# Kernel optimization log

Hardware: AMD Instinct MI355X
Metric: run time of the kernel (lower is better)

The kernel has to match this reference:

```python
import jax, jax.numpy as jnp
import numpy as np

HEAD_DIM = 128
SCALE = 1.0 / np.sqrt(HEAD_DIM).astype(np.float32)


def setup_inputs() -> dict:
    key = jax.random.key(0)
    kq, kk, kv = jax.random.split(key, 3)
    B, S, H, KVH, D = 2, 2048, 32, 8, HEAD_DIM
    q = jax.random.normal(kq, (B, S, H, D), dtype=jnp.float32)
    k = jax.random.normal(kk, (B, S, KVH, D), dtype=jnp.float32)
    v = jax.random.normal(kv, (B, S, KVH, D), dtype=jnp.float32)
    return {"q": q, "k": k, "v": v}


def reference(q, k, v):
    # q: [B,S,H,D]; k,v: [B,S,KVH,D]
    B, S, H, D = q.shape
    kvh = k.shape[2]
    if kvh != H:
        rep = H // kvh
        # repeat_interleave along head dim (GQA -> MHA expansion)
        k = jnp.repeat(k, rep, axis=2)
        v = jnp.repeat(v, rep, axis=2)
    # scores: [B,H,S,S]
    scores = jnp.einsum("bqhd,bkhd->bhqk", q, k) * SCALE
    causal_mask = jnp.triu(jnp.ones((S, S), dtype=bool), k=1)
    scores = jnp.where(causal_mask, -jnp.inf, scores)
    attn = jax.nn.softmax(scores, axis=-1)
    # output back to [B,S,H,D]
    out = jnp.einsum("bhqk,bkhd->bqhd", attn, v)
    return out
```

## Files before the change

kernel.cpp:

```cpp
#include <hip/hip_runtime.h>
#include <hip/hip_bf16.h>
#include <stdint.h>

#define B_    2
#define S_    2048
#define H_    32
#define KVH_  8
#define D_    128
#define NBLK  512
#define NTOT_ 34

typedef __bf16 bf16x8 __attribute__((ext_vector_type(8)));
typedef unsigned short u16x8 __attribute__((ext_vector_type(8)));
typedef unsigned int u32x4 __attribute__((ext_vector_type(4)));
typedef float f32x4 __attribute__((ext_vector_type(4)));

__device__ constexpr float SCALE_LOG2E = 0.08838834764831845f * 1.4426950408889634f;
__device__ constexpr float DEFER_LOG2  = 11.0f;

__device__ __forceinline__ unsigned short f2bf(float f) {
    unsigned int u = __builtin_bit_cast(unsigned int, f);
    u = (u + 0x7FFFu + ((u >> 16) & 1u)) >> 16;
    return (unsigned short)u;
}

__device__ __forceinline__ unsigned int cvt_pk_bf16(float lo, float hi) {
    unsigned int r;
    asm("v_cvt_pk_bf16_f32 %0, %1, %2" : "=v"(r) : "v"(lo), "v"(hi));
    return r;
}

__device__ __forceinline__ void gload16(const unsigned short* gsrc, unsigned short* ldst) {
    __builtin_amdgcn_global_load_lds(
        (const __attribute__((address_space(1))) unsigned int*)gsrc,
        (__attribute__((address_space(3))) unsigned int*)ldst,
        16, 0, 0);
}

__global__ __launch_bounds__(256) void prepass(const float* __restrict__ k,
                                               const float* __restrict__ v,
                                               unsigned short* __restrict__ kbuf,
                                               unsigned short* __restrict__ vbuf) {
    if (blockIdx.x < 2048) {
        int tid = blockIdx.x * 256 + threadIdx.x;
        int l   = tid & 63;
        int ch  = (tid >> 6) & 3;
        int kb  = (tid >> 8) & 127;
        int kvh = (tid >> 15) & 7;
        int b   = tid >> 18;
        int s   = kb * 16 + (l & 15);
        int d0  = ch * 32 + (l >> 4) * 8;
        const float* src = k + (((size_t)b * S_ + s) * KVH_ + kvh) * D_ + d0;
        float4 x = ((const float4*)src)[0];
        float4 y = ((const float4*)src)[1];
        u16x8 o;
        o[0] = f2bf(x.x); o[1] = f2bf(x.y); o[2] = f2bf(x.z); o[3] = f2bf(x.w);
        o[4] = f2bf(y.x); o[5] = f2bf(y.y); o[6] = f2bf(y.z); o[7] = f2bf(y.w);
        *(u16x8*)(kbuf + ((size_t)(((b * KVH_ + kvh) * 128 + kb) * 4 + ch) * 64 + l) * 8) = o;
    } else {
        __shared__ float tile[32][130];
        int bid = blockIdx.x - 2048;
        int vb  = bid & 63;
        int kvh = (bid >> 6) & 7;
        int b   = bid >> 9;
        int t   = threadIdx.x;

        int s   = t >> 3;
        int c16 = (t & 7) * 16;
        const float* src = v + (((size_t)b * S_ + vb * 32 + s) * KVH_ + kvh) * D_ + c16;
        #pragma unroll
        for (int j = 0; j < 4; ++j) {
            float4 x = ((const float4*)src)[j];
            tile[s][c16 + 4 * j + 0] = x.x; tile[s][c16 + 4 * j + 1] = x.y;
            tile[s][c16 + 4 * j + 2] = x.z; tile[s][c16 + 4 * j + 3] = x.w;
        }
        __syncthreads();

        #pragma unroll
        for (int i = 0; i < 2; ++i) {
            int ci = t + i * 256;
            int mt = ci >> 6, l = ci & 63, c = l & 15, g = l >> 4;
            u16x8 o;
            #pragma unroll
            for (int j = 0; j < 8; ++j) o[j] = f2bf(tile[g * 8 + j][mt * 16 + c]);
            *(u16x8*)(vbuf + ((size_t)(((b * KVH_ + kvh) * 64 + vb) * 8 + mt) * 64 + l) * 8) = o;
        }
    }
}

__global__ __launch_bounds__(256, 2)
void attn_fwd(const float* __restrict__ q,
              const unsigned short* __restrict__ kbuf,
              const unsigned short* __restrict__ vbuf,
              float* __restrict__ out)
{
    int pid = blockIdx.x;
    int lid = (pid & 7) * (NBLK / 8) + (pid >> 3);
    int p   = lid & 7;
    int bh  = lid >> 3;
    int b   = bh >> 5, h = bh & 31, kvh = h >> 2;
    const int qtA = 15 - p;
    const int NTA = 2 * qtA + 2;
    const int qtB = p;

    const int tid = threadIdx.x, wave = tid >> 6, lane = tid & 63;
    const int c = lane & 15, g = lane >> 4;

    __shared__ __align__(16) unsigned short ldsK[2][8192];
    __shared__ __align__(16) unsigned short ldsV[2][8192];

    const unsigned short* kfb = kbuf + (size_t)(b * KVH_ + kvh) * (S_ * D_);
    const unsigned short* vfb = vbuf + (size_t)(b * KVH_ + kvh) * (S_ * D_);

    const int addr0 = (c + 16 * ((2 * g) & 3)) * 4;
    const int addr1 = (c + 16 * ((2 * g + 1) & 3)) * 4;
    const bool ghi = (g >= 2);

    auto kvt = [&](int u) { return (u < NTA) ? u : (u - NTA); };
    auto stageK = [&](int u) {
        const unsigned short* ks = kfb + (size_t)kvt(u) * 8192;
        unsigned short* ld = &ldsK[u & 1][0];
        #pragma unroll
        for (int i = 0; i < 4; ++i) {
            int seg = wave * 4 + i;
            gload16(ks + seg * 512 + lane * 8, ld + seg * 512);
        }
    };
    auto stageV = [&](int u) {
        const unsigned short* vs = vfb + (size_t)kvt(u) * 8192;
        unsigned short* ld = &ldsV[u & 1][0];
        #pragma unroll
        for (int i = 0; i < 4; ++i) {
            int seg = wave * 4 + i;
            gload16(vs + seg * 512 + lane * 8, ld + seg * 512);
        }
    };

    stageK(0);
    asm volatile("s_waitcnt vmcnt(0)" ::: "memory");
    __builtin_amdgcn_s_barrier();
    asm volatile("" ::: "memory");

    auto run_tile = [&](int qt, int u0, int NT) {
        const int q0w = qt * 128 + wave * 32;

        bf16x8 qf[2][4];
        #pragma unroll
        for (int m = 0; m < 2; ++m) {
            const float* qp = q + ((size_t)b * S_ + q0w + m * 16 + c) * (H_ * D_) + h * D_ + g * 8;
            #pragma unroll
            for (int ch = 0; ch < 4; ++ch) {
                float4 a  = ((const float4*)(qp + ch * 32))[0];
                float4 bb = ((const float4*)(qp + ch * 32))[1];
                u16x8 tt;
                tt[0] = f2bf(a.x * SCALE_LOG2E);  tt[1] = f2bf(a.y * SCALE_LOG2E);
                tt[2] = f2bf(a.z * SCALE_LOG2E);  tt[3] = f2bf(a.w * SCALE_LOG2E);
                tt[4] = f2bf(bb.x * SCALE_LOG2E); tt[5] = f2bf(bb.y * SCALE_LOG2E);
                tt[6] = f2bf(bb.z * SCALE_LOG2E); tt[7] = f2bf(bb.w * SCALE_LOG2E);
                qf[m][ch] = __builtin_bit_cast(bf16x8, tt);
            }
        }

        f32x4 acc[2][8];
        #pragma unroll
        for (int m = 0; m < 2; ++m)
            #pragma unroll
            for (int mt = 0; mt < 8; ++mt) acc[m][mt] = (f32x4){0.f, 0.f, 0.f, 0.f};
        float mrun[2], lsum[2];
        #pragma unroll
        for (int m = 0; m < 2; ++m) { mrun[m] = -INFINITY; lsum[m] = 0.f; }

        u32x4 pfA[2][2], pfB[2][2];

        auto body = [&](int u, int it, int NT_, auto& pfW, auto& pfR, int ODD) {
            if (u + 1 < NTOT_) stageK(u + 1);
            stageV(u);
            const bool act = (it < NT_ - 1) || (wave >= 2);
            const int k0 = it * 64;
            f32x4 sv[2][4];

            if (act) {
                __builtin_amdgcn_s_setprio(1);
                #pragma unroll
                for (int t2 = 0; t2 < 4; ++t2) {
                    bf16x8 kf[4];
                    #pragma unroll
                    for (int ch = 0; ch < 4; ++ch)
                        kf[ch] = *(const bf16x8*)&ldsK[ODD][(t2 * 4 + ch) * 512 + lane * 8];
                    sv[0][t2] = (f32x4){0.f, 0.f, 0.f, 0.f};
                    sv[1][t2] = (f32x4){0.f, 0.f, 0.f, 0.f};
                    #pragma unroll
                    for (int ch = 0; ch < 4; ++ch) {
                        sv[0][t2] = __builtin_amdgcn_mfma_f32_16x16x32_bf16(kf[ch], qf[0][ch], sv[0][t2], 0, 0, 0);
                        sv[1][t2] = __builtin_amdgcn_mfma_f32_16x16x32_bf16(kf[ch], qf[1][ch], sv[1][t2], 0, 0, 0);
                    }
                }
                __builtin_amdgcn_s_setprio(0);
            }

            if (it > 0) {
                __builtin_amdgcn_s_setprio(1);
                #pragma unroll
                for (int kc = 0; kc < 2; ++kc) {
                    bf16x8 pb0 = __builtin_bit_cast(bf16x8, pfR[0][kc]);
                    bf16x8 pb1 = __builtin_bit_cast(bf16x8, pfR[1][kc]);
                    #pragma unroll
                    for (int mt = 0; mt < 8; ++mt) {
                        bf16x8 vf = *(const bf16x8*)&ldsV[ODD ^ 1][(kc * 8 + mt) * 512 + lane * 8];
                        acc[0][mt] = __builtin_amdgcn_mfma_f32_16x16x32_bf16(vf, pb0, acc[0][mt], 0, 0, 0);
                        acc[1][mt] = __builtin_amdgcn_mfma_f32_16x16x32_bf16(vf, pb1, acc[1][mt], 0, 0, 0);
                    }
                }
                __builtin_amdgcn_s_setprio(0);
            }

            if (act) {
                #pragma unroll
                for (int m = 0; m < 2; ++m) {
                    if (k0 + 63 > q0w + m * 16) {
                        #pragma unroll
                        for (int t2 = 0; t2 < 4; ++t2)
                            #pragma unroll
                            for (int r = 0; r < 4; ++r)
                                if (k0 + 16 * t2 + 4 * g + r > q0w + m * 16 + c) sv[m][t2][r] = -INFINITY;
                    }
                }

                float lm[2];
                #pragma unroll
                for (int m = 0; m < 2; ++m) {
                    float a0 = fmaxf(fmaxf(sv[m][0][0], sv[m][0][1]), fmaxf(sv[m][0][2], sv[m][0][3]));
                    float a1 = fmaxf(fmaxf(sv[m][1][0], sv[m][1][1]), fmaxf(sv[m][1][2], sv[m][1][3]));
                    float a2 = fmaxf(fmaxf(sv[m][2][0], sv[m][2][1]), fmaxf(sv[m][2][2], sv[m][2][3]));
                    float a3 = fmaxf(fmaxf(sv[m][3][0], sv[m][3][1]), fmaxf(sv[m][3][2], sv[m][3][3]));
                    lm[m] = fmaxf(fmaxf(a0, a1), fmaxf(a2, a3));
                }
                bool ok = (lm[0] <= mrun[0] + DEFER_LOG2) && (lm[1] <= mrun[1] + DEFER_LOG2);
                if (!__all(ok)) {
                    #pragma unroll
                    for (int m = 0; m < 2; ++m) {
                        float mx = lm[m];
                        mx = fmaxf(mx, __shfl_xor(mx, 16));
                        mx = fmaxf(mx, __shfl_xor(mx, 32));
                        float mn = fmaxf(mrun[m], mx);
                        float al = exp2f(mrun[m] - mn);
                        mrun[m] = mn;
                        lsum[m] *= al;
                        #pragma unroll
                        for (int mt = 0; mt < 8; ++mt) {
                            acc[m][mt][0] *= al; acc[m][mt][1] *= al;
                            acc[m][mt][2] *= al; acc[m][mt][3] *= al;
                        }
                    }
                }

                #pragma unroll
                for (int m = 0; m < 2; ++m) {
                    float pvv[4][4];
                    #pragma unroll
                    for (int t2 = 0; t2 < 4; ++t2)
                        #pragma unroll
                        for (int r = 0; r < 4; ++r)
                            pvv[t2][r] = exp2f(sv[m][t2][r] - mrun[m]);
                    float s01 = (pvv[0][0] + pvv[0][1]) + (pvv[0][2] + pvv[0][3])
                              + (pvv[1][0] + pvv[1][1]) + (pvv[1][2] + pvv[1][3]);
                    float s23 = (pvv[2][0] + pvv[2][1]) + (pvv[2][2] + pvv[2][3])
                              + (pvv[3][0] + pvv[3][1]) + (pvv[3][2] + pvv[3][3]);
                    lsum[m] += s01 + s23;
                    #pragma unroll
                    for (int kc = 0; kc < 2; ++kc) {
                        unsigned int we0 = cvt_pk_bf16(pvv[2 * kc][0], pvv[2 * kc][1]);
                        unsigned int we1 = cvt_pk_bf16(pvv[2 * kc][2], pvv[2 * kc][3]);
                        unsigned int wo0 = cvt_pk_bf16(pvv[2 * kc + 1][0], pvv[2 * kc + 1][1]);
                        unsigned int wo1 = cvt_pk_bf16(pvv[2 * kc + 1][2], pvv[2 * kc + 1][3]);
                        u32x4 W;
                        {
                            int x0 = __builtin_amdgcn_ds_bpermute(addr0, (int)we0);
                            int x1 = __builtin_amdgcn_ds_bpermute(addr0, (int)wo0);
                            W[0] = (unsigned int)(ghi ? x1 : x0);
                            int x2 = __builtin_amdgcn_ds_bpermute(addr0, (int)we1);
                            int x3 = __builtin_amdgcn_ds_bpermute(addr0, (int)wo1);
                            W[1] = (unsigned int)(ghi ? x3 : x2);
                            int x4 = __builtin_amdgcn_ds_bpermute(addr1, (int)we0);
                            int x5 = __builtin_amdgcn_ds_bpermute(addr1, (int)wo0);
                            W[2] = (unsigned int)(ghi ? x5 : x4);
                            int x6 = __builtin_amdgcn_ds_bpermute(addr1, (int)we1);
                            int x7 = __builtin_amdgcn_ds_bpermute(addr1, (int)wo1);
                            W[3] = (unsigned int)(ghi ? x7 : x6);
                        }
                        pfW[m][kc] = W;
                    }
                }
            }

            asm volatile("s_waitcnt vmcnt(0)" ::: "memory");
            __builtin_amdgcn_s_barrier();
            asm volatile("" ::: "memory");
        };

        for (int it = 0; it < NT; it += 2) {
            body(u0 + it,     it,     NT, pfA, pfB, 0);
            body(u0 + it + 1, it + 1, NT, pfB, pfA, 1);
        }

        if (wave >= 2) {
            #pragma unroll
            for (int kc = 0; kc < 2; ++kc) {
                bf16x8 pb0 = __builtin_bit_cast(bf16x8, pfB[0][kc]);
                bf16x8 pb1 = __builtin_bit_cast(bf16x8, pfB[1][kc]);
                #pragma unroll
                for (int mt = 0; mt < 8; ++mt) {
                    bf16x8 vf = *(const bf16x8*)&ldsV[1][(kc * 8 + mt) * 512 + lane * 8];
                    acc[0][mt] = __builtin_amdgcn_mfma_f32_16x16x32_bf16(vf, pb0, acc[0][mt], 0, 0, 0);
                    acc[1][mt] = __builtin_amdgcn_mfma_f32_16x16x32_bf16(vf, pb1, acc[1][mt], 0, 0, 0);
                }
            }
        }

        #pragma unroll
        for (int m = 0; m < 2; ++m) {
            lsum[m] += __shfl_xor(lsum[m], 16);
            lsum[m] += __shfl_xor(lsum[m], 32);
        }
        #pragma unroll
        for (int m = 0; m < 2; ++m) {
            float linv = 1.0f / lsum[m];
            float* ob = out + ((size_t)b * S_ + q0w + m * 16 + c) * (H_ * D_) + h * D_;
            #pragma unroll
            for (int mt = 0; mt < 8; ++mt) {
                float4 o;
                o.x = acc[m][mt][0] * linv; o.y = acc[m][mt][1] * linv;
                o.z = acc[m][mt][2] * linv; o.w = acc[m][mt][3] * linv;
                *(float4*)(ob + mt * 16 + 4 * g) = o;
            }
        }
    };

    run_tile(qtA, 0, NTA);
    run_tile(qtB, NTA, NTOT_ - NTA);
}

extern "C" void kernel_launch(void* const* d_in, const int* in_sizes, int n_in,
                              void* d_out, int out_size, void* d_ws, size_t ws_size,
                              hipStream_t stream) {
    const float* q = (const float*)d_in[0];
    const float* k = (const float*)d_in[1];
    const float* v = (const float*)d_in[2];
    float* out = (float*)d_out;

    unsigned short* kbuf = (unsigned short*)d_ws;
    unsigned short* vbuf = kbuf + (size_t)B_ * KVH_ * S_ * D_;

    prepass<<<3072, 256, 0, stream>>>(k, v, kbuf, vbuf);
    attn_fwd<<<NBLK, 256, 0, stream>>>(q, kbuf, vbuf, out);
}
```

Measured before the change: 128.5 us.

## Use 512-thread blocks with 256-row query tiles instead of paired 128-row tiles

Each block now runs 8 waves over one 256-row query tile, where before it ran 4 waves over two complementary 128-row tiles. Each K/V tile staged in LDS is therefore shared by twice as many waves, and the two-tile causal load balancing gives way to a reversed block order across the two halves of the grid. Per-wave skipping of fully masked tiles (act/pact) replaces the old last-iteration rule. In exchange there is more causal imbalance inside a block, since early waves sit idle at barriers while later waves finish. The launch bounds are raised to 512 threads with 4 blocks per CU, which may constrain registers.

```diff
diff --git a/kernel.cpp b/kernel.cpp
--- a/kernel.cpp
+++ b/kernel.cpp
@@ -8,7 +8,6 @@
 #define KVH_  8
 #define D_    128
 #define NBLK  512
-#define NTOT_ 34
 
 typedef __bf16 bf16x8 __attribute__((ext_vector_type(8)));
 typedef unsigned short u16x8 __attribute__((ext_vector_type(8)));
@@ -88,23 +87,26 @@
     }
 }
 
-__global__ __launch_bounds__(256, 2)
+__global__ __launch_bounds__(512, 4)
 void attn_fwd(const float* __restrict__ q,
               const unsigned short* __restrict__ kbuf,
               const unsigned short* __restrict__ vbuf,
               float* __restrict__ out)
 {
-    int pid = blockIdx.x;
-    int lid = (pid & 7) * (NBLK / 8) + (pid >> 3);
-    int p   = lid & 7;
-    int bh  = lid >> 3;
-    int b   = bh >> 5, h = bh & 31, kvh = h >> 2;
-    const int qtA = 15 - p;
-    const int NTA = 2 * qtA + 2;
-    const int qtB = p;
+    const int pid  = blockIdx.x;
+    const int half = pid >> 8;
+    const int r    = pid & 255;
+    const int kvg  = r & 15;
+    const int hq   = (r >> 4) & 3;
+    const int j    = r >> 6;
+    const int b    = kvg >> 3, kvh = kvg & 7;
+    const int h    = kvh * 4 + hq;
+    const int qt   = half ? j : 7 - j;
+    const int NT   = 4 * qt + 4;
 
     const int tid = threadIdx.x, wave = tid >> 6, lane = tid & 63;
     const int c = lane & 15, g = lane >> 4;
+    const int q0w = qt * 256 + wave * 32;
 
     __shared__ __align__(16) unsigned short ldsK[2][8192];
     __shared__ __align__(16) unsigned short ldsV[2][8192];
@@ -116,22 +118,21 @@
     const int addr1 = (c + 16 * ((2 * g + 1) & 3)) * 4;
     const bool ghi = (g >= 2);
 
-    auto kvt = [&](int u) { return (u < NTA) ? u : (u - NTA); };
     auto stageK = [&](int u) {
-        const unsigned short* ks = kfb + (size_t)kvt(u) * 8192;
+        const unsigned short* ks = kfb + (size_t)u * 8192;
         unsigned short* ld = &ldsK[u & 1][0];
         #pragma unroll
-        for (int i = 0; i < 4; ++i) {
-            int seg = wave * 4 + i;
+        for (int i = 0; i < 2; ++i) {
+            int seg = wave * 2 + i;
             gload16(ks + seg * 512 + lane * 8, ld + seg * 512);
         }
     };
     auto stageV = [&](int u) {
-        const unsigned short* vs = vfb + (size_t)kvt(u) * 8192;
+        const unsigned short* vs = vfb + (size_t)u * 8192;
         unsigned short* ld = &ldsV[u & 1][0];
         #pragma unroll
-        for (int i = 0; i < 4; ++i) {
-            int seg = wave * 4 + i;
+        for (int i = 0; i < 2; ++i) {
+            int seg = wave * 2 + i;
             gload16(vs + seg * 512 + lane * 8, ld + seg * 512);
         }
     };
@@ -141,203 +142,197 @@
     __builtin_amdgcn_s_barrier();
     asm volatile("" ::: "memory");
 
-    auto run_tile = [&](int qt, int u0, int NT) {
-        const int q0w = qt * 128 + wave * 32;
-
-        bf16x8 qf[2][4];
-        #pragma unroll
-        for (int m = 0; m < 2; ++m) {
-            const float* qp = q + ((size_t)b * S_ + q0w + m * 16 + c) * (H_ * D_) + h * D_ + g * 8;
-            #pragma unroll
-            for (int ch = 0; ch < 4; ++ch) {
-                float4 a  = ((const float4*)(qp + ch * 32))[0];
-                float4 bb = ((const float4*)(qp + ch * 32))[1];
-                u16x8 tt;
-                tt[0] = f2bf(a.x * SCALE_LOG2E);  tt[1] = f2bf(a.y * SCALE_LOG2E);
-                tt[2] = f2bf(a.z * SCALE_LOG2E);  tt[3] = f2bf(a.w * SCALE_LOG2E);
-                tt[4] = f2bf(bb.x * SCALE_LOG2E); tt[5] = f2bf(bb.y * SCALE_LOG2E);
-                tt[6] = f2bf(bb.z * SCALE_LOG2E); tt[7] = f2bf(bb.w * SCALE_LOG2E);
-                qf[m][ch] = __builtin_bit_cast(bf16x8, tt);
-            }
-        }
-
-        f32x4 acc[2][8];
-        #pragma unroll
-        for (int m = 0; m < 2; ++m)
-            #pragma unroll
-            for (int mt = 0; mt < 8; ++mt) acc[m][mt] = (f32x4){0.f, 0.f, 0.f, 0.f};
-        float mrun[2], lsum[2];
-        #pragma unroll
-        for (int m = 0; m < 2; ++m) { mrun[m] = -INFINITY; lsum[m] = 0.f; }
-
-        u32x4 pfA[2][2], pfB[2][2];
-
-        auto body = [&](int u, int it, int NT_, auto& pfW, auto& pfR, int ODD) {
-            if (u + 1 < NTOT_) stageK(u + 1);
-            stageV(u);
-            const bool act = (it < NT_ - 1) || (wave >= 2);
-            const int k0 = it * 64;
-            f32x4 sv[2][4];
-
-            if (act) {
-                __builtin_amdgcn_s_setprio(1);
-                #pragma unroll
-                for (int t2 = 0; t2 < 4; ++t2) {
-                    bf16x8 kf[4];
-                    #pragma unroll
-                    for (int ch = 0; ch < 4; ++ch)
-                        kf[ch] = *(const bf16x8*)&ldsK[ODD][(t2 * 4 + ch) * 512 + lane * 8];
-                    sv[0][t2] = (f32x4){0.f, 0.f, 0.f, 0.f};
-                    sv[1][t2] = (f32x4){0.f, 0.f, 0.f, 0.f};
-                    #pragma unroll
-                    for (int ch = 0; ch < 4; ++ch) {
-                        sv[0][t2] = __builtin_amdgcn_mfma_f32_16x16x32_bf16(kf[ch], qf[0][ch], sv[0][t2], 0, 0, 0);
-                        sv[1][t2] = __builtin_amdgcn_mfma_f32_16x16x32_bf16(kf[ch], qf[1][ch], sv[1][t2], 0, 0, 0);
-                    }
-                }
-                __builtin_amdgcn_s_setprio(0);
-            }
-
-            if (it > 0) {
-                __builtin_amdgcn_s_setprio(1);
-                #pragma unroll
-                for (int kc = 0; kc < 2; ++kc) {
-                    bf16x8 pb0 = __builtin_bit_cast(bf16x8, pfR[0][kc]);
-                    bf16x8 pb1 = __builtin_bit_cast(bf16x8, pfR[1][kc]);
-                    #pragma unroll
-                    for (int mt = 0; mt < 8; ++mt) {
-                        bf16x8 vf = *(const bf16x8*)&ldsV[ODD ^ 1][(kc * 8 + mt) * 512 + lane * 8];
-                        acc[0][mt] = __builtin_amdgcn_mfma_f32_16x16x32_bf16(vf, pb0, acc[0][mt], 0, 0, 0);
-                        acc[1][mt] = __builtin_amdgcn_mfma_f32_16x16x32_bf16(vf, pb1, acc[1][mt], 0, 0, 0);
-                    }
-                }
-                __builtin_amdgcn_s_setprio(0);
-            }
-
-            if (act) {
-                #pragma unroll
-                for (int m = 0; m < 2; ++m) {
-                    if (k0 + 63 > q0w + m * 16) {
-                        #pragma unroll
-                        for (int t2 = 0; t2 < 4; ++t2)
-                            #pragma unroll
-                            for (int r = 0; r < 4; ++r)
-                                if (k0 + 16 * t2 + 4 * g + r > q0w + m * 16 + c) sv[m][t2][r] = -INFINITY;
-                    }
-                }
-
-                float lm[2];
-                #pragma unroll
-                for (int m = 0; m < 2; ++m) {
-                    float a0 = fmaxf(fmaxf(sv[m][0][0], sv[m][0][1]), fmaxf(sv[m][0][2], sv[m][0][3]));
-                    float a1 = fmaxf(fmaxf(sv[m][1][0], sv[m][1][1]), fmaxf(sv[m][1][2], sv[m][1][3]));
-                    float a2 = fmaxf(fmaxf(sv[m][2][0], sv[m][2][1]), fmaxf(sv[m][2][2], sv[m][2][3]));
-                    float a3 = fmaxf(fmaxf(sv[m][3][0], sv[m][3][1]), fmaxf(sv[m][3][2], sv[m][3][3]));
-                    lm[m] = fmaxf(fmaxf(a0, a1), fmaxf(a2, a3));
-                }
-                bool ok = (lm[0] <= mrun[0] + DEFER_LOG2) && (lm[1] <= mrun[1] + DEFER_LOG2);
-                if (!__all(ok)) {
-                    #pragma unroll
-                    for (int m = 0; m < 2; ++m) {
-                        float mx = lm[m];
-                        mx = fmaxf(mx, __shfl_xor(mx, 16));
-                        mx = fmaxf(mx, __shfl_xor(mx, 32));
-                        float mn = fmaxf(mrun[m], mx);
-                        float al = exp2f(mrun[m] - mn);
-                        mrun[m] = mn;
-                        lsum[m] *= al;
-                        #pragma unroll
-                        for (int mt = 0; mt < 8; ++mt) {
-                            acc[m][mt][0] *= al; acc[m][mt][1] *= al;
-                            acc[m][mt][2] *= al; acc[m][mt][3] *= al;
-                        }
-                    }
-                }
-
-                #pragma unroll
-                for (int m = 0; m < 2; ++m) {
-                    float pvv[4][4];
+    bf16x8 qf[2][4];
+    #pragma unroll
+    for (int m = 0; m < 2; ++m) {
+        const float* qp = q + ((size_t)b * S_ + q0w + m * 16 + c) * (H_ * D_) + h * D_ + g * 8;
+        #pragma unroll
+        for (int ch = 0; ch < 4; ++ch) {
+            float4 a  = ((const float4*)(qp + ch * 32))[0];
+            float4 bb = ((const float4*)(qp + ch * 32))[1];
+            u16x8 tt;
+            tt[0] = f2bf(a.x * SCALE_LOG2E);  tt[1] = f2bf(a.y * SCALE_LOG2E);
+            tt[2] = f2bf(a.z * SCALE_LOG2E);  tt[3] = f2bf(a.w * SCALE_LOG2E);
+            tt[4] = f2bf(bb.x * SCALE_LOG2E); tt[5] = f2bf(bb.y * SCALE_LOG2E);
+            tt[6] = f2bf(bb.z * SCALE_LOG2E); tt[7] = f2bf(bb.w * SCALE_LOG2E);
+            qf[m][ch] = __builtin_bit_cast(bf16x8, tt);
+        }
+    }
+
+    f32x4 acc[2][8];
+    #pragma unroll
+    for (int m = 0; m < 2; ++m)
+        #pragma unroll
+        for (int mt = 0; mt < 8; ++mt) acc[m][mt] = (f32x4){0.f, 0.f, 0.f, 0.f};
+    float mrun[2], lsum[2];
+    #pragma unroll
+    for (int m = 0; m < 2; ++m) { mrun[m] = -INFINITY; lsum[m] = 0.f; }
+
+    u32x4 pfA[2][2], pfB[2][2];
+
+    auto body = [&](int it, auto& pfW, auto& pfR, int ODD) {
+        if (it + 1 < NT) stageK(it + 1);
+        stageV(it);
+        const int k0 = it * 64;
+        const bool act  = (k0 <= q0w + 31);
+        const bool pact = (it > 0) && (k0 - 64 <= q0w + 31);
+        f32x4 sv[2][4];
+
+        if (act) {
+            __builtin_amdgcn_s_setprio(1);
+            #pragma unroll
+            for (int t2 = 0; t2 < 4; ++t2) {
+                bf16x8 kf[4];
+                #pragma unroll
+                for (int ch = 0; ch < 4; ++ch)
+                    kf[ch] = *(const bf16x8*)&ldsK[ODD][(t2 * 4 + ch) * 512 + lane * 8];
+                sv[0][t2] = (f32x4){0.f, 0.f, 0.f, 0.f};
+                sv[1][t2] = (f32x4){0.f, 0.f, 0.f, 0.f};
+                #pragma unroll
+                for (int ch = 0; ch < 4; ++ch) {
+                    sv[0][t2] = __builtin_amdgcn_mfma_f32_16x16x32_bf16(kf[ch], qf[0][ch], sv[0][t2], 0, 0, 0);
+                    sv[1][t2] = __builtin_amdgcn_mfma_f32_16x16x32_bf16(kf[ch], qf[1][ch], sv[1][t2], 0, 0, 0);
+                }
+            }
+            __builtin_amdgcn_s_setprio(0);
+        }
+
+        if (pact) {
+            __builtin_amdgcn_s_setprio(1);
+            #pragma unroll
+            for (int kc = 0; kc < 2; ++kc) {
+                bf16x8 pb0 = __builtin_bit_cast(bf16x8, pfR[0][kc]);
+                bf16x8 pb1 = __builtin_bit_cast(bf16x8, pfR[1][kc]);
+                #pragma unroll
+                for (int mt = 0; mt < 8; ++mt) {
+                    bf16x8 vf = *(const bf16x8*)&ldsV[ODD ^ 1][(kc * 8 + mt) * 512 + lane * 8];
+                    acc[0][mt] = __builtin_amdgcn_mfma_f32_16x16x32_bf16(vf, pb0, acc[0][mt], 0, 0, 0);
+                    acc[1][mt] = __builtin_amdgcn_mfma_f32_16x16x32_bf16(vf, pb1, acc[1][mt], 0, 0, 0);
+                }
+            }
+            __builtin_amdgcn_s_setprio(0);
+        }
+
+        if (act) {
+            #pragma unroll
+            for (int m = 0; m < 2; ++m) {
+                if (k0 + 63 > q0w + m * 16) {
                     #pragma unroll
                     for (int t2 = 0; t2 < 4; ++t2)
                         #pragma unroll
-                        for (int r = 0; r < 4; ++r)
-                            pvv[t2][r] = exp2f(sv[m][t2][r] - mrun[m]);
-                    float s01 = (pvv[0][0] + pvv[0][1]) + (pvv[0][2] + pvv[0][3])
-                              + (pvv[1][0] + pvv[1][1]) + (pvv[1][2] + pvv[1][3]);
-                    float s23 = (pvv[2][0] + pvv[2][1]) + (pvv[2][2] + pvv[2][3])
-                              + (pvv[3][0] + pvv[3][1]) + (pvv[3][2] + pvv[3][3]);
-                    lsum[m] += s01 + s23;
+                        for (int rr = 0; rr < 4; ++rr)
+                            if (k0 + 16 * t2 + 4 * g + rr > q0w + m * 16 + c) sv[m][t2][rr] = -INFINITY;
+                }
+            }
+
+            float lm[2];
+            #pragma unroll
+            for (int m = 0; m < 2; ++m) {
+                float a0 = fmaxf(fmaxf(sv[m][0][0], sv[m][0][1]), fmaxf(sv[m][0][2], sv[m][0][3]));
+                float a1 = fmaxf(fmaxf(sv[m][1][0], sv[m][1][1]), fmaxf(sv[m][1][2], sv[m][1][3]));
+                float a2 = fmaxf(fmaxf(sv[m][2][0], sv[m][2][1]), fmaxf(sv[m][2][2], sv[m][2][3]));
+                float a3 = fmaxf(fmaxf(sv[m][3][0], sv[m][3][1]), fmaxf(sv[m][3][2], sv[m][3][3]));
+                lm[m] = fmaxf(fmaxf(a0, a1), fmaxf(a2, a3));
+            }
+            bool ok = (lm[0] <= mrun[0] + DEFER_LOG2) && (lm[1] <= mrun[1] + DEFER_LOG2);
+            if (!__all(ok)) {
+                #pragma unroll
+                for (int m = 0; m < 2; ++m) {
+                    float mx = lm[m];
+                    mx = fmaxf(mx, __shfl_xor(mx, 16));
+                    mx = fmaxf(mx, __shfl_xor(mx, 32));
+                    float mn = fmaxf(mrun[m], mx);
+                    float al = exp2f(mrun[m] - mn);
+                    mrun[m] = mn;
+                    lsum[m] *= al;
                     #pragma unroll
-                    for (int kc = 0; kc < 2; ++kc) {
-                        unsigned int we0 = cvt_pk_bf16(pvv[2 * kc][0], pvv[2 * kc][1]);
-                        unsigned int we1 = cvt_pk_bf16(pvv[2 * kc][2], pvv[2 * kc][3]);
-                        unsigned int wo0 = cvt_pk_bf16(pvv[2 * kc + 1][0], pvv[2 * kc + 1][1]);
-                        unsigned int wo1 = cvt_pk_bf16(pvv[2 * kc + 1][2], pvv[2 * kc + 1][3]);
-                        u32x4 W;
-                        {
-                            int x0 = __builtin_amdgcn_ds_bpermute(addr0, (int)we0);
-                            int x1 = __builtin_amdgcn_ds_bpermute(addr0, (int)wo0);
-                            W[0] = (unsigned int)(ghi ? x1 : x0);
-                            int x2 = __builtin_amdgcn_ds_bpermute(addr0, (int)we1);
-                            int x3 = __builtin_amdgcn_ds_bpermute(addr0, (int)wo1);
-                            W[1] = (unsigned int)(ghi ? x3 : x2);
-                            int x4 = __builtin_amdgcn_ds_bpermute(addr1, (int)we0);
-                            int x5 = __builtin_amdgcn_ds_bpermute(addr1, (int)wo0);
-                            W[2] = (unsigned int)(ghi ? x5 : x4);
-                            int x6 = __builtin_amdgcn_ds_bpermute(addr1, (int)we1);
-                            int x7 = __builtin_amdgcn_ds_bpermute(addr1, (int)wo1);
-                            W[3] = (unsigned int)(ghi ? x7 : x6);
-                        }
-                        pfW[m][kc] = W;
+                    for (int mt = 0; mt < 8; ++mt) {
+                        acc[m][mt][0] *= al; acc[m][mt][1] *= al;
+                        acc[m][mt][2] *= al; acc[m][mt][3] *= al;
                     }
                 }
             }
 
-            asm volatile("s_waitcnt vmcnt(0)" ::: "memory");
-            __builtin_amdgcn_s_barrier();
-            asm volatile("" ::: "memory");
-        };
-
-        for (int it = 0; it < NT; it += 2) {
-            body(u0 + it,     it,     NT, pfA, pfB, 0);
-            body(u0 + it + 1, it + 1, NT, pfB, pfA, 1);
-        }
-
-        if (wave >= 2) {
-            #pragma unroll
-            for (int kc = 0; kc < 2; ++kc) {
-                bf16x8 pb0 = __builtin_bit_cast(bf16x8, pfB[0][kc]);
-                bf16x8 pb1 = __builtin_bit_cast(bf16x8, pfB[1][kc]);
-                #pragma unroll
-                for (int mt = 0; mt < 8; ++mt) {
-                    bf16x8 vf = *(const bf16x8*)&ldsV[1][(kc * 8 + mt) * 512 + lane * 8];
-                    acc[0][mt] = __builtin_amdgcn_mfma_f32_16x16x32_bf16(vf, pb0, acc[0][mt], 0, 0, 0);
-                    acc[1][mt] = __builtin_amdgcn_mfma_f32_16x16x32_bf16(vf, pb1, acc[1][mt], 0, 0, 0);
-                }
-            }
-        }
-
-        #pragma unroll
-        for (int m = 0; m < 2; ++m) {
-            lsum[m] += __shfl_xor(lsum[m], 16);
-            lsum[m] += __shfl_xor(lsum[m], 32);
-        }
-        #pragma unroll
-        for (int m = 0; m < 2; ++m) {
-            float linv = 1.0f / lsum[m];
-            float* ob = out + ((size_t)b * S_ + q0w + m * 16 + c) * (H_ * D_) + h * D_;
+            #pragma unroll
+            for (int m = 0; m < 2; ++m) {
+                float pvv[4][4];
+                #pragma unroll
+                for (int t2 = 0; t2 < 4; ++t2)
+                    #pragma unroll
+                    for (int rr = 0; rr < 4; ++rr)
+                        pvv[t2][rr] = exp2f(sv[m][t2][rr] - mrun[m]);
+                float s01 = (pvv[0][0] + pvv[0][1]) + (pvv[0][2] + pvv[0][3])
+                          + (pvv[1][0] + pvv[1][1]) + (pvv[1][2] + pvv[1][3]);
+                float s23 = (pvv[2][0] + pvv[2][1]) + (pvv[2][2] + pvv[2][3])
+                          + (pvv[3][0] + pvv[3][1]) + (pvv[3][2] + pvv[3][3]);
+                lsum[m] += s01 + s23;
+                #pragma unroll
+                for (int kc = 0; kc < 2; ++kc) {
+                    unsigned int we0 = cvt_pk_bf16(pvv[2 * kc][0], pvv[2 * kc][1]);
+                    unsigned int we1 = cvt_pk_bf16(pvv[2 * kc][2], pvv[2 * kc][3]);
+                    unsigned int wo0 = cvt_pk_bf16(pvv[2 * kc + 1][0], pvv[2 * kc + 1][1]);
+                    unsigned int wo1 = cvt_pk_bf16(pvv[2 * kc + 1][2], pvv[2 * kc + 1][3]);
+                    u32x4 W;
+                    {
+                        int x0 = __builtin_amdgcn_ds_bpermute(addr0, (int)we0);
+                        int x1 = __builtin_amdgcn_ds_bpermute(addr0, (int)wo0);
+                        W[0] = (unsigned int)(ghi ? x1 : x0);
+                        int x2 = __builtin_amdgcn_ds_bpermute(addr0, (int)we1);
+                        int x3 = __builtin_amdgcn_ds_bpermute(addr0, (int)wo1);
+                        W[1] = (unsigned int)(ghi ? x3 : x2);
+                        int x4 = __builtin_amdgcn_ds_bpermute(addr1, (int)we0);
+                        int x5 = __builtin_amdgcn_ds_bpermute(addr1, (int)wo0);
+                        W[2] = (unsigned int)(ghi ? x5 : x4);
+                        int x6 = __builtin_amdgcn_ds_bpermute(addr1, (int)we1);
+                        int x7 = __builtin_amdgcn_ds_bpermute(addr1, (int)wo1);
+                        W[3] = (unsigned int)(ghi ? x7 : x6);
+                    }
+                    pfW[m][kc] = W;
+                }
+            }
+        }
+
+        asm volatile("s_waitcnt vmcnt(0)" ::: "memory");
+        __builtin_amdgcn_s_barrier();
+        asm volatile("" ::: "memory");
+    };
+
+    for (int it = 0; it < NT; it += 2) {
+        body(it,     pfA, pfB, 0);
+        body(it + 1, pfB, pfA, 1);
+    }
+
+    if (wave >= 6) {
+        #pragma unroll
+        for (int kc = 0; kc < 2; ++kc) {
+            bf16x8 pb0 = __builtin_bit_cast(bf16x8, pfB[0][kc]);
+            bf16x8 pb1 = __builtin_bit_cast(bf16x8, pfB[1][kc]);
             #pragma unroll
             for (int mt = 0; mt < 8; ++mt) {
-                float4 o;
-                o.x = acc[m][mt][0] * linv; o.y = acc[m][mt][1] * linv;
-                o.z = acc[m][mt][2] * linv; o.w = acc[m][mt][3] * linv;
-                *(float4*)(ob + mt * 16 + 4 * g) = o;
-            }
-        }
-    };
-
-    run_tile(qtA, 0, NTA);
-    run_tile(qtB, NTA, NTOT_ - NTA);
+                bf16x8 vf = *(const bf16x8*)&ldsV[1][(kc * 8 + mt) * 512 + lane * 8];
+                acc[0][mt] = __builtin_amdgcn_mfma_f32_16x16x32_bf16(vf, pb0, acc[0][mt], 0, 0, 0);
+                acc[1][mt] = __builtin_amdgcn_mfma_f32_16x16x32_bf16(vf, pb1, acc[1][mt], 0, 0, 0);
+            }
+        }
+    }
+
+    #pragma unroll
+    for (int m = 0; m < 2; ++m) {
+        lsum[m] += __shfl_xor(lsum[m], 16);
+        lsum[m] += __shfl_xor(lsum[m], 32);
+    }
+    #pragma unroll
+    for (int m = 0; m < 2; ++m) {
+        float linv = 1.0f / lsum[m];
+        float* ob = out + ((size_t)b * S_ + q0w + m * 16 + c) * (H_ * D_) + h * D_;
+        #pragma unroll
+        for (int mt = 0; mt < 8; ++mt) {
+            float4 o;
+            o.x = acc[m][mt][0] * linv; o.y = acc[m][mt][1] * linv;
+            o.z = acc[m][mt][2] * linv; o.w = acc[m][mt][3] * linv;
+            *(float4*)(ob + mt * 16 + 4 * g) = o;
+        }
+    }
 }
 
 extern "C" void kernel_launch(void* const* d_in, const int* in_sizes, int n_in,
@@ -352,5 +347,5 @@
     unsigned short* vbuf = kbuf + (size_t)B_ * KVH_ * S_ * D_;
 
     prepass<<<3072, 256, 0, stream>>>(k, v, kbuf, vbuf);
-    attn_fwd<<<NBLK, 256, 0, stream>>>(q, kbuf, vbuf, out);
-}
+    attn_fwd<<<NBLK, 512, 0, stream>>>(q, kbuf, vbuf, out);
+}
```

Measured after the change: 440.7 us. +242.9%, slower.

## Switch attention MFMAs from 16x16x32 to 32x32x16 with matching K/V layouts

Applied to the files above, without the earlier changes.

Replaces the 16x16x32 bf16 MFMA tiling with 32x32x16 MFMAs for both QK^T and PV. The prepass packing of K and V is reworked to match the new operand layout, and the P-fragment shuffle is simplified to a single lane^32 bpermute. Per-tile activity is now computed from actual causal bounds rather than a wave heuristic. The aim is fewer MFMA issues, fewer LDS reads and fewer permutes per tile, at the cost of larger accumulator register footprints that may pressure occupancy.

```diff
diff --git a/kernel.cpp b/kernel.cpp
--- a/kernel.cpp
+++ b/kernel.cpp
@@ -13,7 +13,7 @@
 typedef __bf16 bf16x8 __attribute__((ext_vector_type(8)));
 typedef unsigned short u16x8 __attribute__((ext_vector_type(8)));
 typedef unsigned int u32x4 __attribute__((ext_vector_type(4)));
-typedef float f32x4 __attribute__((ext_vector_type(4)));
+typedef float f32x16 __attribute__((ext_vector_type(16)));
 
 __device__ constexpr float SCALE_LOG2E = 0.08838834764831845f * 1.4426950408889634f;
 __device__ constexpr float DEFER_LOG2  = 11.0f;
@@ -44,46 +44,50 @@
     if (blockIdx.x < 2048) {
         int tid = blockIdx.x * 256 + threadIdx.x;
         int l   = tid & 63;
-        int ch  = (tid >> 6) & 3;
-        int kb  = (tid >> 8) & 127;
+        int ch  = (tid >> 6) & 7;
+        int kt  = (tid >> 9) & 63;
         int kvh = (tid >> 15) & 7;
-        int b   = tid >> 18;
-        int s   = kb * 16 + (l & 15);
-        int d0  = ch * 32 + (l >> 4) * 8;
+        int b   = (tid >> 18) & 1;
+        int s   = kt * 32 + (l & 31);
+        int d0  = ch * 16 + (l >> 5) * 8;
         const float* src = k + (((size_t)b * S_ + s) * KVH_ + kvh) * D_ + d0;
         float4 x = ((const float4*)src)[0];
         float4 y = ((const float4*)src)[1];
         u16x8 o;
         o[0] = f2bf(x.x); o[1] = f2bf(x.y); o[2] = f2bf(x.z); o[3] = f2bf(x.w);
         o[4] = f2bf(y.x); o[5] = f2bf(y.y); o[6] = f2bf(y.z); o[7] = f2bf(y.w);
-        *(u16x8*)(kbuf + ((size_t)(((b * KVH_ + kvh) * 128 + kb) * 4 + ch) * 64 + l) * 8) = o;
+        *(u16x8*)(kbuf + ((size_t)(((b * KVH_ + kvh) * 64 + kt) * 8 + ch) * 512 + l * 8)) = o;
     } else {
-        __shared__ float tile[32][130];
+        __shared__ float tile[64][132];
         int bid = blockIdx.x - 2048;
-        int vb  = bid & 63;
-        int kvh = (bid >> 6) & 7;
-        int b   = bid >> 9;
+        int u   = bid & 31;
+        int kvh = (bid >> 5) & 7;
+        int b   = bid >> 8;
         int t   = threadIdx.x;
 
-        int s   = t >> 3;
-        int c16 = (t & 7) * 16;
-        const float* src = v + (((size_t)b * S_ + vb * 32 + s) * KVH_ + kvh) * D_ + c16;
-        #pragma unroll
-        for (int j = 0; j < 4; ++j) {
-            float4 x = ((const float4*)src)[j];
-            tile[s][c16 + 4 * j + 0] = x.x; tile[s][c16 + 4 * j + 1] = x.y;
-            tile[s][c16 + 4 * j + 2] = x.z; tile[s][c16 + 4 * j + 3] = x.w;
+        int s  = t >> 2;
+        int cb = (t & 3) * 32;
+        const float* src = v + (((size_t)b * S_ + u * 64 + s) * KVH_ + kvh) * D_ + cb;
+        #pragma unroll
+        for (int i = 0; i < 8; ++i) {
+            float4 x = ((const float4*)src)[i];
+            tile[s][cb + 4 * i + 0] = x.x; tile[s][cb + 4 * i + 1] = x.y;
+            tile[s][cb + 4 * i + 2] = x.z; tile[s][cb + 4 * i + 3] = x.w;
         }
         __syncthreads();
 
         #pragma unroll
-        for (int i = 0; i < 2; ++i) {
-            int ci = t + i * 256;
-            int mt = ci >> 6, l = ci & 63, c = l & 15, g = l >> 4;
+        for (int i = 0; i < 4; ++i) {
+            int slot = t + 256 * i;
+            int ci = slot >> 6;
+            int l  = slot & 63;
+            int kk = ci >> 2, dt = ci & 3;
+            int h2 = l >> 5;
             u16x8 o;
             #pragma unroll
-            for (int j = 0; j < 8; ++j) o[j] = f2bf(tile[g * 8 + j][mt * 16 + c]);
-            *(u16x8*)(vbuf + ((size_t)(((b * KVH_ + kvh) * 64 + vb) * 8 + mt) * 64 + l) * 8) = o;
+            for (int j = 0; j < 8; ++j)
+                o[j] = f2bf(tile[kk * 16 + h2 * 8 + j][dt * 32 + (l & 31)]);
+            *(u16x8*)(vbuf + ((size_t)(((b * KVH_ + kvh) * 32 + u) * 16 + ci) * 512 + l * 8)) = o;
         }
     }
 }
@@ -104,17 +108,14 @@
     const int qtB = p;
 
     const int tid = threadIdx.x, wave = tid >> 6, lane = tid & 63;
-    const int c = lane & 15, g = lane >> 4;
+    const int c32 = lane & 31, hi = lane >> 5;
+    const int addrx = ((lane ^ 32) << 2);
 
     __shared__ __align__(16) unsigned short ldsK[2][8192];
     __shared__ __align__(16) unsigned short ldsV[2][8192];
 
     const unsigned short* kfb = kbuf + (size_t)(b * KVH_ + kvh) * (S_ * D_);
     const unsigned short* vfb = vbuf + (size_t)(b * KVH_ + kvh) * (S_ * D_);
-
-    const int addr0 = (c + 16 * ((2 * g) & 3)) * 4;
-    const int addr1 = (c + 16 * ((2 * g + 1) & 3)) * 4;
-    const bool ghi = (g >= 2);
 
     auto kvt = [&](int u) { return (u < NTA) ? u : (u - NTA); };
     auto stageK = [&](int u) {
@@ -144,151 +145,128 @@
     auto run_tile = [&](int qt, int u0, int NT) {
         const int q0w = qt * 128 + wave * 32;
 
-        bf16x8 qf[2][4];
-        #pragma unroll
-        for (int m = 0; m < 2; ++m) {
-            const float* qp = q + ((size_t)b * S_ + q0w + m * 16 + c) * (H_ * D_) + h * D_ + g * 8;
-            #pragma unroll
-            for (int ch = 0; ch < 4; ++ch) {
-                float4 a  = ((const float4*)(qp + ch * 32))[0];
-                float4 bb = ((const float4*)(qp + ch * 32))[1];
+        bf16x8 qf[8];
+        {
+            const float* qp = q + ((size_t)b * S_ + q0w + c32) * (H_ * D_) + h * D_ + hi * 8;
+            #pragma unroll
+            for (int ch = 0; ch < 8; ++ch) {
+                float4 a  = ((const float4*)(qp + ch * 16))[0];
+                float4 bb = ((const float4*)(qp + ch * 16))[1];
                 u16x8 tt;
                 tt[0] = f2bf(a.x * SCALE_LOG2E);  tt[1] = f2bf(a.y * SCALE_LOG2E);
                 tt[2] = f2bf(a.z * SCALE_LOG2E);  tt[3] = f2bf(a.w * SCALE_LOG2E);
                 tt[4] = f2bf(bb.x * SCALE_LOG2E); tt[5] = f2bf(bb.y * SCALE_LOG2E);
                 tt[6] = f2bf(bb.z * SCALE_LOG2E); tt[7] = f2bf(bb.w * SCALE_LOG2E);
-                qf[m][ch] = __builtin_bit_cast(bf16x8, tt);
-            }
-        }
-
-        f32x4 acc[2][8];
-        #pragma unroll
-        for (int m = 0; m < 2; ++m)
-            #pragma unroll
-            for (int mt = 0; mt < 8; ++mt) acc[m][mt] = (f32x4){0.f, 0.f, 0.f, 0.f};
-        float mrun[2], lsum[2];
-        #pragma unroll
-        for (int m = 0; m < 2; ++m) { mrun[m] = -INFINITY; lsum[m] = 0.f; }
-
-        u32x4 pfA[2][2], pfB[2][2];
-
-        auto body = [&](int u, int it, int NT_, auto& pfW, auto& pfR, int ODD) {
+                qf[ch] = __builtin_bit_cast(bf16x8, tt);
+            }
+        }
+
+        f32x16 acc[4];
+        #pragma unroll
+        for (int dt = 0; dt < 4; ++dt)
+            #pragma unroll
+            for (int i = 0; i < 16; ++i) acc[dt][i] = 0.f;
+        float mrun = -INFINITY, lsum = 0.f;
+
+        u32x4 pfA[4], pfB[4];
+
+        auto body = [&](int u, int it, int NT_, u32x4 (&pfW)[4], u32x4 (&pfR)[4], int ODD) {
             if (u + 1 < NTOT_) stageK(u + 1);
             stageV(u);
-            const bool act = (it < NT_ - 1) || (wave >= 2);
             const int k0 = it * 64;
-            f32x4 sv[2][4];
+            const bool act  = (k0 <= q0w + 31);
+            const bool pact = (it > 0) && (k0 - 64 <= q0w + 31);
+            f32x16 sv[2];
 
             if (act) {
+                #pragma unroll
+                for (int kt = 0; kt < 2; ++kt)
+                    #pragma unroll
+                    for (int i = 0; i < 16; ++i) sv[kt][i] = 0.f;
                 __builtin_amdgcn_s_setprio(1);
                 #pragma unroll
-                for (int t2 = 0; t2 < 4; ++t2) {
-                    bf16x8 kf[4];
-                    #pragma unroll
-                    for (int ch = 0; ch < 4; ++ch)
-                        kf[ch] = *(const bf16x8*)&ldsK[ODD][(t2 * 4 + ch) * 512 + lane * 8];
-                    sv[0][t2] = (f32x4){0.f, 0.f, 0.f, 0.f};
-                    sv[1][t2] = (f32x4){0.f, 0.f, 0.f, 0.f};
-                    #pragma unroll
-                    for (int ch = 0; ch < 4; ++ch) {
-                        sv[0][t2] = __builtin_amdgcn_mfma_f32_16x16x32_bf16(kf[ch], qf[0][ch], sv[0][t2], 0, 0, 0);
-                        sv[1][t2] = __builtin_amdgcn_mfma_f32_16x16x32_bf16(kf[ch], qf[1][ch], sv[1][t2], 0, 0, 0);
+                for (int ch = 0; ch < 8; ++ch) {
+                    bf16x8 kf0 = *(const bf16x8*)&ldsK[ODD][(0 * 8 + ch) * 512 + lane * 8];
+                    bf16x8 kf1 = *(const bf16x8*)&ldsK[ODD][(1 * 8 + ch) * 512 + lane * 8];
+                    sv[0] = __builtin_amdgcn_mfma_f32_32x32x16_bf16(kf0, qf[ch], sv[0], 0, 0, 0);
+                    sv[1] = __builtin_amdgcn_mfma_f32_32x32x16_bf16(kf1, qf[ch], sv[1], 0, 0, 0);
+                }
+                __builtin_amdgcn_s_setprio(0);
+            }
+
+            if (pact) {
+                __builtin_amdgcn_s_setprio(1);
+                #pragma unroll
+                for (int kk = 0; kk < 4; ++kk) {
+                    bf16x8 pb = __builtin_bit_cast(bf16x8, pfR[kk]);
+                    #pragma unroll
+                    for (int dt = 0; dt < 4; ++dt) {
+                        bf16x8 vf = *(const bf16x8*)&ldsV[ODD ^ 1][(kk * 4 + dt) * 512 + lane * 8];
+                        acc[dt] = __builtin_amdgcn_mfma_f32_32x32x16_bf16(vf, pb, acc[dt], 0, 0, 0);
                     }
                 }
                 __builtin_amdgcn_s_setprio(0);
             }
 
-            if (it > 0) {
-                __builtin_amdgcn_s_setprio(1);
-                #pragma unroll
-                for (int kc = 0; kc < 2; ++kc) {
-                    bf16x8 pb0 = __builtin_bit_cast(bf16x8, pfR[0][kc]);
-                    bf16x8 pb1 = __builtin_bit_cast(bf16x8, pfR[1][kc]);
-                    #pragma unroll
-                    for (int mt = 0; mt < 8; ++mt) {
-                        bf16x8 vf = *(const bf16x8*)&ldsV[ODD ^ 1][(kc * 8 + mt) * 512 + lane * 8];
-                        acc[0][mt] = __builtin_amdgcn_mfma_f32_16x16x32_bf16(vf, pb0, acc[0][mt], 0, 0, 0);
-                        acc[1][mt] = __builtin_amdgcn_mfma_f32_16x16x32_bf16(vf, pb1, acc[1][mt], 0, 0, 0);
+            if (act) {
+                if (k0 + 63 > q0w) {
+                    #pragma unroll
+                    for (int kt = 0; kt < 2; ++kt)
+                        #pragma unroll
+                        for (int r = 0; r < 16; ++r) {
+                            int key = k0 + 32 * kt + (r & 3) + 8 * (r >> 2) + 4 * hi;
+                            if (key > q0w + c32) sv[kt][r] = -INFINITY;
+                        }
+                }
+
+                float lm = sv[0][0];
+                #pragma unroll
+                for (int r = 1; r < 16; ++r) lm = fmaxf(lm, sv[0][r]);
+                #pragma unroll
+                for (int r = 0; r < 16; ++r) lm = fmaxf(lm, sv[1][r]);
+                bool ok = (lm <= mrun + DEFER_LOG2);
+                if (!__all(ok)) {
+                    float mx = fmaxf(lm, __shfl_xor(lm, 32));
+                    float mn = fmaxf(mrun, mx);
+                    float al = exp2f(mrun - mn);
+                    mrun = mn;
+                    lsum *= al;
+                    #pragma unroll
+                    for (int dt = 0; dt < 4; ++dt)
+                        #pragma unroll
+                        for (int i = 0; i < 16; ++i) acc[dt][i] *= al;
+                }
+
+                float pp[2][16];
+                float sacc = 0.f;
+                #pragma unroll
+                for (int kt = 0; kt < 2; ++kt)
+                    #pragma unroll
+                    for (int r = 0; r < 16; ++r) {
+                        pp[kt][r] = exp2f(sv[kt][r] - mrun);
+                        sacc += pp[kt][r];
                     }
-                }
-                __builtin_amdgcn_s_setprio(0);
-            }
-
-            if (act) {
-                #pragma unroll
-                for (int m = 0; m < 2; ++m) {
-                    if (k0 + 63 > q0w + m * 16) {
-                        #pragma unroll
-                        for (int t2 = 0; t2 < 4; ++t2)
-                            #pragma unroll
-                            for (int r = 0; r < 4; ++r)
-                                if (k0 + 16 * t2 + 4 * g + r > q0w + m * 16 + c) sv[m][t2][r] = -INFINITY;
-                    }
-                }
-
-                float lm[2];
-                #pragma unroll
-                for (int m = 0; m < 2; ++m) {
-                    float a0 = fmaxf(fmaxf(sv[m][0][0], sv[m][0][1]), fmaxf(sv[m][0][2], sv[m][0][3]));
-                    float a1 = fmaxf(fmaxf(sv[m][1][0], sv[m][1][1]), fmaxf(sv[m][1][2], sv[m][1][3]));
-                    float a2 = fmaxf(fmaxf(sv[m][2][0], sv[m][2][1]), fmaxf(sv[m][2][2], sv[m][2][3]));
-                    float a3 = fmaxf(fmaxf(sv[m][3][0], sv[m][3][1]), fmaxf(sv[m][3][2], sv[m][3][3]));
-                    lm[m] = fmaxf(fmaxf(a0, a1), fmaxf(a2, a3));
-                }
-                bool ok = (lm[0] <= mrun[0] + DEFER_LOG2) && (lm[1] <= mrun[1] + DEFER_LOG2);
-                if (!__all(ok)) {
-                    #pragma unroll
-                    for (int m = 0; m < 2; ++m) {
-                        float mx = lm[m];
-                        mx = fmaxf(mx, __shfl_xor(mx, 16));
-                        mx = fmaxf(mx, __shfl_xor(mx, 32));
-                        float mn = fmaxf(mrun[m], mx);
-                        float al = exp2f(mrun[m] - mn);
-                        mrun[m] = mn;
-                        lsum[m] *= al;
-                        #pragma unroll
-                        for (int mt = 0; mt < 8; ++mt) {
-                            acc[m][mt][0] *= al; acc[m][mt][1] *= al;
-                            acc[m][mt][2] *= al; acc[m][mt][3] *= al;
-                        }
-                    }
-                }
-
-                #pragma unroll
-                for (int m = 0; m < 2; ++m) {
-                    float pvv[4][4];
-                    #pragma unroll
-                    for (int t2 = 0; t2 < 4; ++t2)
-                        #pragma unroll
-                        for (int r = 0; r < 4; ++r)
-                            pvv[t2][r] = exp2f(sv[m][t2][r] - mrun[m]);
-                    float s01 = (pvv[0][0] + pvv[0][1]) + (pvv[0][2] + pvv[0][3])
-                              + (pvv[1][0] + pvv[1][1]) + (pvv[1][2] + pvv[1][3]);
-                    float s23 = (pvv[2][0] + pvv[2][1]) + (pvv[2][2] + pvv[2][3])
-                              + (pvv[3][0] + pvv[3][1]) + (pvv[3][2] + pvv[3][3]);
-                    lsum[m] += s01 + s23;
-                    #pragma unroll
-                    for (int kc = 0; kc < 2; ++kc) {
-                        unsigned int we0 = cvt_pk_bf16(pvv[2 * kc][0], pvv[2 * kc][1]);
-                        unsigned int we1 = cvt_pk_bf16(pvv[2 * kc][2], pvv[2 * kc][3]);
-                        unsigned int wo0 = cvt_pk_bf16(pvv[2 * kc + 1][0], pvv[2 * kc + 1][1]);
-                        unsigned int wo1 = cvt_pk_bf16(pvv[2 * kc + 1][2], pvv[2 * kc + 1][3]);
+                lsum += sacc;
+
+                #pragma unroll
+                for (int kt = 0; kt < 2; ++kt) {
+                    #pragma unroll
+                    for (int kap = 0; kap < 2; ++kap) {
+                        int base = kap * 8;
+                        unsigned int U0 = cvt_pk_bf16(pp[kt][base + 0], pp[kt][base + 1]);
+                        unsigned int U1 = cvt_pk_bf16(pp[kt][base + 2], pp[kt][base + 3]);
+                        unsigned int V0 = cvt_pk_bf16(pp[kt][base + 4], pp[kt][base + 5]);
+                        unsigned int V1 = cvt_pk_bf16(pp[kt][base + 6], pp[kt][base + 7]);
+                        unsigned int U0x = (unsigned int)__builtin_amdgcn_ds_bpermute(addrx, (int)U0);
+                        unsigned int U1x = (unsigned int)__builtin_amdgcn_ds_bpermute(addrx, (int)U1);
+                        unsigned int V0x = (unsigned int)__builtin_amdgcn_ds_bpermute(addrx, (int)V0);
+                        unsigned int V1x = (unsigned int)__builtin_amdgcn_ds_bpermute(addrx, (int)V1);
                         u32x4 W;
-                        {
-                            int x0 = __builtin_amdgcn_ds_bpermute(addr0, (int)we0);
-                            int x1 = __builtin_amdgcn_ds_bpermute(addr0, (int)wo0);
-                            W[0] = (unsigned int)(ghi ? x1 : x0);
-                            int x2 = __builtin_amdgcn_ds_bpermute(addr0, (int)we1);
-                            int x3 = __builtin_amdgcn_ds_bpermute(addr0, (int)wo1);
-                            W[1] = (unsigned int)(ghi ? x3 : x2);
-                            int x4 = __builtin_amdgcn_ds_bpermute(addr1, (int)we0);
-                            int x5 = __builtin_amdgcn_ds_bpermute(addr1, (int)wo0);
-                            W[2] = (unsigned int)(ghi ? x5 : x4);
-                            int x6 = __builtin_amdgcn_ds_bpermute(addr1, (int)we1);
-                            int x7 = __builtin_amdgcn_ds_bpermute(addr1, (int)wo1);
-                            W[3] = (unsigned int)(ghi ? x7 : x6);
-                        }
-                        pfW[m][kc] = W;
+                        W[0] = hi ? V0x : U0;
+                        W[1] = hi ? V1x : U1;
+                        W[2] = hi ? V0 : U0x;
+                        W[3] = hi ? V1 : U1x;
+                        pfW[kt * 2 + kap] = W;
                     }
                 }
             }
@@ -305,35 +283,30 @@
 
         if (wave >= 2) {
             #pragma unroll
-            for (int kc = 0; kc < 2; ++kc) {
-                bf16x8 pb0 = __builtin_bit_cast(bf16x8, pfB[0][kc]);
-                bf16x8 pb1 = __builtin_bit_cast(bf16x8, pfB[1][kc]);
-                #pragma unroll
-                for (int mt = 0; mt < 8; ++mt) {
-                    bf16x8 vf = *(const bf16x8*)&ldsV[1][(kc * 8 + mt) * 512 + lane * 8];
-                    acc[0][mt] = __builtin_amdgcn_mfma_f32_16x16x32_bf16(vf, pb0, acc[0][mt], 0, 0, 0);
-                    acc[1][mt] = __builtin_amdgcn_mfma_f32_16x16x32_bf16(vf, pb1, acc[1][mt], 0, 0, 0);
-                }
-            }
-        }
-
-        #pragma unroll
-        for (int m = 0; m < 2; ++m) {
-            lsum[m] += __shfl_xor(lsum[m], 16);
-            lsum[m] += __shfl_xor(lsum[m], 32);
-        }
-        #pragma unroll
-        for (int m = 0; m < 2; ++m) {
-            float linv = 1.0f / lsum[m];
-            float* ob = out + ((size_t)b * S_ + q0w + m * 16 + c) * (H_ * D_) + h * D_;
-            #pragma unroll
-            for (int mt = 0; mt < 8; ++mt) {
+            for (int kk = 0; kk < 4; ++kk) {
+                bf16x8 pb = __builtin_bit_cast(bf16x8, pfB[kk]);
+                #pragma unroll
+                for (int dt = 0; dt < 4; ++dt) {
+                    bf16x8 vf = *(const bf16x8*)&ldsV[1][(kk * 4 + dt) * 512 + lane * 8];
+                    acc[dt] = __builtin_amdgcn_mfma_f32_32x32x16_bf16(vf, pb, acc[dt], 0, 0, 0);
+                }
+            }
+        }
+
+        lsum += __shfl_xor(lsum, 32);
+        float linv = 1.0f / lsum;
+        float* ob = out + ((size_t)b * S_ + q0w + c32) * (H_ * D_) + h * D_;
+        #pragma unroll
+        for (int dt = 0; dt < 4; ++dt)
+            #pragma unroll
+            for (int rq = 0; rq < 4; ++rq) {
                 float4 o;
-                o.x = acc[m][mt][0] * linv; o.y = acc[m][mt][1] * linv;
-                o.z = acc[m][mt][2] * linv; o.w = acc[m][mt][3] * linv;
-                *(float4*)(ob + mt * 16 + 4 * g) = o;
-            }
-        }
+                o.x = acc[dt][4 * rq + 0] * linv;
+                o.y = acc[dt][4 * rq + 1] * linv;
+                o.z = acc[dt][4 * rq + 2] * linv;
+                o.w = acc[dt][4 * rq + 3] * linv;
+                *(float4*)(ob + dt * 32 + rq * 8 + hi * 4) = o;
+            }
     };
 
     run_tile(qtA, 0, NTA);
@@ -351,6 +324,6 @@
     unsigned short* kbuf = (unsigned short*)d_ws;
     unsigned short* vbuf = kbuf + (size_t)B_ * KVH_ * S_ * D_;
 
-    prepass<<<3072, 256, 0, stream>>>(k, v, kbuf, vbuf);
+    prepass<<<2560, 256, 0, stream>>>(k, v, kbuf, vbuf);
     attn_fwd<<<NBLK, 256, 0, stream>>>(q, kbuf, vbuf, out);
 }
```

Result: faster. 123.9 us (-3.6%).
